# Kernel tuning notes

Hardware: AMD Instinct MI355X
Metric: run time of the kernel (lower is better)

Reference implementation:

```python
import jax, jax.numpy as jnp
import numpy as np

B, T, E, H, V = 64, 160, 512, 1024, 32000


def setup_inputs() -> dict:
    key = jax.random.key(0)
    ks = jax.random.split(key, 8)
    s = 1.0 / np.sqrt(H).astype(np.float32)
    return {
        "contexts": jax.random.randint(ks[0], (B, T), 0, V),
        "responses": jax.random.randint(ks[1], (B, T), 0, V),
        "emb": jax.random.normal(ks[2], (V, E), jnp.float32) * 0.02,
        "Wih": jax.random.uniform(ks[3], (4 * H, E), jnp.float32, -s, s),
        "Whh": jax.random.uniform(ks[4], (4 * H, H), jnp.float32, -s, s),
        "bih": jax.random.uniform(ks[5], (4 * H,), jnp.float32, -s, s),
        "bhh": jax.random.uniform(ks[6], (4 * H,), jnp.float32, -s, s),
        "M": jax.random.normal(ks[7], (H, H), jnp.float32),
    }


def _lstm_final_h(tokens, emb, Wih, Whh, bih, bhh):
    """Single-layer LSTM (PyTorch gate order i,f,g,o); returns final hidden state [B,H]."""
    x = emb[tokens]                      # [B, T, E]
    b = bih + bhh                        # [4H]
    hdim = Whh.shape[1]

    def step(carry, xt):
        h, c = carry
        gates = xt @ Wih.T + h @ Whh.T + b          # [B, 4H]
        i, f, g, o = jnp.split(gates, 4, axis=-1)
        c = jax.nn.sigmoid(f) * c + jax.nn.sigmoid(i) * jnp.tanh(g)
        h = jax.nn.sigmoid(o) * jnp.tanh(c)
        return (h, c), None

    h0 = jnp.zeros((tokens.shape[0], hdim), x.dtype)
    (h, _), _ = jax.lax.scan(step, (h0, h0), jnp.swapaxes(x, 0, 1))  # scan over time
    return h


def reference(contexts, responses, emb, Wih, Whh, bih, bhh, M):
    ch = _lstm_final_h(contexts, emb, Wih, Whh, bih, bhh)   # [B, H]
    rh = _lstm_final_h(responses, emb, Wih, Whh, bih, bhh)  # [B, H]
    # batched bilinear: sigmoid(diag(C @ M @ R^T)) -- replaces the per-example Python loop
    return jax.nn.sigmoid(jnp.einsum('bi,ij,bj->b', ch, M, rh))
```

## Files before the change

kernel.cpp:

```cpp
#include <hip/hip_runtime.h>
#include <math.h>


#define BB 64
#define TT 160
#define EE 512
#define HH 1024
#define G4 4096
#define ROWS 128
#define NB 256

typedef unsigned short u16;
typedef unsigned int u32;
typedef __attribute__((ext_vector_type(8))) __bf16 bf16x8;
typedef __attribute__((ext_vector_type(8))) short short8;
typedef __attribute__((ext_vector_type(4))) short short4v;
typedef __attribute__((ext_vector_type(4))) float f32x4;

__device__ __forceinline__ u16 f2b(float f) {
    unsigned u = __float_as_uint(f);
    u = u + 0x7fffu + ((u >> 16) & 1u);
    return (u16)(u >> 16);
}
__device__ __forceinline__ float b2f(u16 s) { return __uint_as_float(((unsigned)s) << 16); }

__device__ __forceinline__ f32x4 mfma16(short8 a, short8 b, f32x4 c) {
    return __builtin_amdgcn_mfma_f32_16x16x32_bf16(
        __builtin_bit_cast(bf16x8, a), __builtin_bit_cast(bf16x8, b), c, 0, 0, 0);
}

__device__ __forceinline__ void g2l16(const void* gsrc, void* ldst) {
    __builtin_amdgcn_global_load_lds(
        (const __attribute__((address_space(1))) u32*)gsrc,
        (__attribute__((address_space(3))) u32*)ldst, 16, 0, 0);
}

__global__ __launch_bounds__(256) void cvt_kernel(const float* __restrict__ in,
                                                  u16* __restrict__ out, int n4) {
    int i = blockIdx.x * 256 + threadIdx.x;
    if (i < n4) {
        f32x4 v = *(const f32x4*)(in + (size_t)i * 4);
        short4v o;
        o.x = (short)f2b(v.x); o.y = (short)f2b(v.y);
        o.z = (short)f2b(v.z); o.w = (short)f2b(v.w);
        *(short4v*)(out + (size_t)i * 4) = o;
    }
}

__global__ __launch_bounds__(256) void pre_gemm2(
    const int* __restrict__ ctx, const int* __restrict__ rsp,
    const u16* __restrict__ embb, const u16* __restrict__ Wihb,
    const float* __restrict__ bih, const float* __restrict__ bhh,
    u16* __restrict__ xg)
{
    __shared__ __align__(16) u16 As[2][128][64];
    __shared__ __align__(16) u16 Ws[2][128][64];
    __shared__ int toks[128];
    const int tid = threadIdx.x;
    const int n0 = blockIdx.x * 128;
    const int t  = blockIdx.y;

    if (tid < 128) {
        int r = tid;
        toks[tid] = (r < BB) ? ctx[r * TT + t] : rsp[(r - BB) * TT + t];
    }
    __syncthreads();

    const u16* asrc[4]; const u16* bsrc[4];
    #pragma unroll
    for (int q = 0; q < 4; ++q) {
        int i = tid + q * 256;
        int row = i >> 3, c16 = i & 7;
        int scol = ((c16 ^ (row & 7)) * 8);
        asrc[q] = embb + (size_t)toks[row] * EE + scol;
        bsrc[q] = Wihb + (size_t)(n0 + row) * EE + scol;
    }

    const int lane = tid & 63, wave = tid >> 6;
    const int wr = (wave >> 1) * 64, wc = (wave & 1) * 64;
    const int l15 = lane & 15, l4 = lane >> 4;
    f32x4 acc[4][4] = {};

    #pragma unroll
    for (int q = 0; q < 4; ++q) {
        g2l16(asrc[q], (char*)&As[0][0][0] + (tid + q * 256) * 16);
        g2l16(bsrc[q], (char*)&Ws[0][0][0] + (tid + q * 256) * 16);
    }
    for (int it = 0; it < 8; ++it) {
        __syncthreads();
        if (it + 1 < 8) {
            int kk = (it + 1) * 64, bs = (it + 1) & 1;
            #pragma unroll
            for (int q = 0; q < 4; ++q) {
                g2l16(asrc[q] + kk, (char*)&As[bs][0][0] + (tid + q * 256) * 16);
                g2l16(bsrc[q] + kk, (char*)&Ws[bs][0][0] + (tid + q * 256) * 16);
            }
        }
        const int b = it & 1;
        #pragma unroll
        for (int ks = 0; ks < 2; ++ks) {
            int c16 = ks * 4 + l4;
            short8 a[4], w[4];
            #pragma unroll
            for (int mf = 0; mf < 4; ++mf) {
                int R = wr + mf * 16 + l15;
                a[mf] = *(const short8*)((const char*)&As[b][0][0] + R * 128 + ((c16 ^ (R & 7)) << 4));
            }
            #pragma unroll
            for (int nf = 0; nf < 4; ++nf) {
                int Nn = wc + nf * 16 + l15;
                w[nf] = *(const short8*)((const char*)&Ws[b][0][0] + Nn * 128 + ((c16 ^ (Nn & 7)) << 4));
            }
            #pragma unroll
            for (int mf = 0; mf < 4; ++mf)
                #pragma unroll
                for (int nf = 0; nf < 4; ++nf)
                    acc[mf][nf] = mfma16(a[mf], w[nf], acc[mf][nf]);
        }
    }

    u16* xp = xg + (size_t)t * ROWS * G4;
    #pragma unroll
    for (int nf = 0; nf < 4; ++nf) {
        int n = n0 + wc + nf * 16 + l15;
        float bias = bih[n] + bhh[n];
        #pragma unroll
        for (int mf = 0; mf < 4; ++mf)
            #pragma unroll
            for (int q = 0; q < 4; ++q) {
                int r = wr + mf * 16 + l4 * 4 + q;
                xp[(size_t)r * G4 + n] = f2b(acc[mf][nf][q] + bias);
            }
    }
}

__global__ __launch_bounds__(512) void lstm_persist2(
    const u16* __restrict__ Whhb, const u16* __restrict__ xg,
    u16* __restrict__ hbuf, unsigned* __restrict__ bar)
{
    __shared__ float G[2][2][32][33];

    const int tid = threadIdx.x;
    const int bx = blockIdx.x;
    const int cg = bx & 127, rg = bx >> 7;
    const int r0 = rg * 64, j0 = cg * 8;

    const int lane = tid & 63, wave = tid >> 6;
    const int rsub = wave >> 2;
    const int kh   = wave & 3;
    const int l15 = lane & 15, l4 = lane >> 4;

    short8 breg[2][8];
    #pragma unroll
    for (int nf = 0; nf < 2; ++nf) {
        int c = nf * 16 + l15;
        int n = (c >> 3) * HH + j0 + (c & 7);
        const u16* wp = Whhb + (size_t)n * HH + kh * 256 + l4 * 8;
        #pragma unroll
        for (int ks = 0; ks < 8; ++ks)
            breg[nf][ks] = *(const short8*)(wp + ks * 32);
    }

    const int ur = tid >> 2;
    const int uj = (tid & 3) * 2;
    float c0 = 0.f, c1 = 0.f;

    __syncthreads();

    for (int t = 0; t < TT; ++t) {
        const u16* hin = hbuf + (size_t)(t & 1) * ROWS * HH;
        u16* hout      = hbuf + (size_t)((t + 1) & 1) * ROWS * HH;

        u32 xv[4] = {0, 0, 0, 0};
        if (tid < 256) {
            const u16* xp = xg + ((size_t)t * ROWS + r0 + ur) * G4 + j0 + uj;
            #pragma unroll
            for (int q = 0; q < 4; ++q) xv[q] = *(const u32*)(xp + q * HH);
        }

        const u16* abase = hin + (size_t)(r0 + rsub * 32 + l15) * HH + kh * 256 + l4 * 8;
        short8 a[2][8];
        #pragma unroll
        for (int half = 0; half < 2; ++half)
            #pragma unroll
            for (int ks = 0; ks < 8; ++ks)
                asm volatile("global_load_dwordx4 %0, %1, off sc0 sc1"
                             : "=v"(a[half][ks])
                             : "v"(abase + half * 16 * HH + ks * 32));
        asm volatile("s_waitcnt vmcnt(0)" ::: "memory");
        __builtin_amdgcn_sched_barrier(0);

        f32x4 acc[2][2] = {};
        #pragma unroll
        for (int ks = 0; ks < 8; ++ks) {
            acc[0][0] = mfma16(a[0][ks], breg[0][ks], acc[0][0]);
            acc[0][1] = mfma16(a[0][ks], breg[1][ks], acc[0][1]);
            acc[1][0] = mfma16(a[1][ks], breg[0][ks], acc[1][0]);
            acc[1][1] = mfma16(a[1][ks], breg[1][ks], acc[1][1]);
        }

        if (kh < 2) {
            #pragma unroll
            for (int mf = 0; mf < 2; ++mf)
                #pragma unroll
                for (int nf = 0; nf < 2; ++nf)
                    #pragma unroll
                    for (int q = 0; q < 4; ++q)
                        G[kh][rsub][mf * 16 + l4 * 4 + q][nf * 16 + l15] = acc[mf][nf][q];
        }
        __syncthreads();
        if (kh >= 2) {
            #pragma unroll
            for (int mf = 0; mf < 2; ++mf)
                #pragma unroll
                for (int nf = 0; nf < 2; ++nf)
                    #pragma unroll
                    for (int q = 0; q < 4; ++q)
                        G[kh - 2][rsub][mf * 16 + l4 * 4 + q][nf * 16 + l15] += acc[mf][nf][q];
        }
        __syncthreads();

        if (tid < 256) {
            const int rs = ur >> 5, rl = ur & 31;
            float g0[4], g1[4];
            #pragma unroll
            for (int q = 0; q < 4; ++q) {
                float x0 = b2f((u16)(xv[q] & 0xffffu));
                float x1 = b2f((u16)(xv[q] >> 16));
                g0[q] = G[0][rs][rl][q * 8 + uj]     + G[1][rs][rl][q * 8 + uj]     + x0;
                g1[q] = G[0][rs][rl][q * 8 + uj + 1] + G[1][rs][rl][q * 8 + uj + 1] + x1;
            }
            float i0 = 1.f / (1.f + expf(-g0[0])), i1 = 1.f / (1.f + expf(-g1[0]));
            float f0 = 1.f / (1.f + expf(-g0[1])), f1 = 1.f / (1.f + expf(-g1[1]));
            float t0 = tanhf(g0[2]),               t1 = tanhf(g1[2]);
            float o0 = 1.f / (1.f + expf(-g0[3])), o1 = 1.f / (1.f + expf(-g1[3]));
            c0 = f0 * c0 + i0 * t0;
            c1 = f1 * c1 + i1 * t1;
            float h0 = o0 * tanhf(c0), h1 = o1 * tanhf(c1);
            u32 hp = (u32)f2b(h0) | ((u32)f2b(h1) << 16);
            u16* hptr = hout + (size_t)(r0 + ur) * HH + j0 + uj;
            asm volatile("global_store_dword %0, %1, off sc0 sc1"
                         :: "v"(hptr), "v"(hp) : "memory");
        }

        if (t < TT - 1) {
            asm volatile("s_waitcnt vmcnt(0)" ::: "memory");
            __syncthreads();
            if (tid == 0) {
                __hip_atomic_fetch_add(bar, 1u, __ATOMIC_RELAXED, __HIP_MEMORY_SCOPE_AGENT);
                unsigned target = (unsigned)(t + 1) * (unsigned)NB;
                long spins = 0;
                while (__hip_atomic_load(bar, __ATOMIC_RELAXED, __HIP_MEMORY_SCOPE_AGENT) < target) {
                    __builtin_amdgcn_s_sleep(1);
                    if (++spins > 20000000L) break;
                }
            }
            __syncthreads();
            __builtin_amdgcn_sched_barrier(0);
        }
    }
}

template<int MODE>
__global__ __launch_bounds__(256) void step_fused(
    const int* __restrict__ ctx, const int* __restrict__ rsp,
    const u16* __restrict__ embb, const u16* __restrict__ Wihb,
    const u16* __restrict__ Whhb, const u16* __restrict__ xg,
    const float* __restrict__ bih, const float* __restrict__ bhh,
    const u16* __restrict__ hin, u16* __restrict__ hout,
    float* __restrict__ c_ws, int t)
{
    __shared__ __align__(16) u16 As[2][64][64];
    __shared__ __align__(16) u16 Ws[2][32][64];
    __shared__ float gs[64][32];
    __shared__ int toks[64];

    const int tid = threadIdx.x;
    const int cg = blockIdx.x & 127, rg = blockIdx.x >> 7;
    const int r0 = rg * 64, j0 = cg * 8;

    if (MODE == 1) {
        if (tid < 64) {
            int r = r0 + tid;
            toks[tid] = (r < BB) ? ctx[r * TT + t] : rsp[(r - BB) * TT + t];
        }
        __syncthreads();
    }

    const int arow0 = tid >> 3, c16a = tid & 7;
    const int arow1 = arow0 + 32;
    const int acol0 = ((c16a ^ (arow0 & 7)) * 8);
    const int acol1 = ((c16a ^ (arow1 & 7)) * 8);
    const u16* hA0 = hin + (size_t)(r0 + arow0) * HH + acol0;
    const u16* hA1 = hin + (size_t)(r0 + arow1) * HH + acol1;
    const u16* eA0 = nullptr; const u16* eA1 = nullptr;
    if (MODE == 1) {
        eA0 = embb + (size_t)toks[arow0] * EE + acol0;
        eA1 = embb + (size_t)toks[arow1] * EE + acol1;
    }
    const int nn = tid >> 3, c16b = tid & 7;
    const int bcol = ((c16b ^ (nn & 7)) * 8);
    const int wrow = (nn >> 3) * HH + j0 + (nn & 7);
    const u16* wHh = Whhb + (size_t)wrow * HH + bcol;
    const u16* wIh = (MODE == 1) ? (Wihb + (size_t)wrow * EE + bcol) : nullptr;

    const int NK = (MODE == 1) ? 24 : 16;

    auto stage = [&](int bs, int it) {
        int kk = it * 64;
        const u16 *s0, *s1, *sw;
        if (MODE == 1 && kk < EE) {
            s0 = eA0 + kk; s1 = eA1 + kk; sw = wIh + kk;
        } else {
            int khh = (MODE == 1) ? kk - EE : kk;
            s0 = hA0 + khh; s1 = hA1 + khh; sw = wHh + khh;
        }
        g2l16(s0, (char*)&As[bs][0][0] + tid * 16);
        g2l16(s1, (char*)&As[bs][0][0] + (tid + 256) * 16);
        g2l16(sw, (char*)&Ws[bs][0][0] + tid * 16);
    };

    const int lane = tid & 63, wave = tid >> 6;
    const int wr = wave * 16;
    const int l15 = lane & 15, l4 = lane >> 4;
    f32x4 acc[2] = {};

    stage(0, 0);
    for (int it = 0; it < NK; ++it) {
        __syncthreads();
        if (it + 1 < NK) stage((it + 1) & 1, it + 1);
        const int b = it & 1;
        #pragma unroll
        for (int ks = 0; ks < 2; ++ks) {
            int c16 = ks * 4 + l4;
            int R = wr + l15;
            short8 a = *(const short8*)((const char*)&As[b][0][0] + R * 128 + ((c16 ^ (R & 7)) << 4));
            #pragma unroll
            for (int nf = 0; nf < 2; ++nf) {
                int Nn = nf * 16 + l15;
                short8 w = *(const short8*)((const char*)&Ws[b][0][0] + Nn * 128 + ((c16 ^ (Nn & 7)) << 4));
                acc[nf] = mfma16(a, w, acc[nf]);
            }
        }
    }
    __syncthreads();
    #pragma unroll
    for (int nf = 0; nf < 2; ++nf)
        #pragma unroll
        for (int q = 0; q < 4; ++q)
            gs[wr + l4 * 4 + q][nf * 16 + l15] = acc[nf][q];
    __syncthreads();

    const int e = tid * 2;
    const int row = e >> 3, jj = e & 7;
    const int rglob = r0 + row;
    float g0[4], g1[4];
    #pragma unroll
    for (int g = 0; g < 4; ++g) { g0[g] = gs[row][g * 8 + jj]; g1[g] = gs[row][g * 8 + jj + 1]; }
    if (MODE == 2) {
        const u16* xp = xg + ((size_t)t * ROWS + rglob) * G4 + j0 + jj;
        #pragma unroll
        for (int g = 0; g < 4; ++g) { g0[g] += b2f(xp[g * HH]); g1[g] += b2f(xp[g * HH + 1]); }
    } else {
        #pragma unroll
        for (int g = 0; g < 4; ++g) {
            int n = g * HH + j0 + jj;
            g0[g] += bih[n] + bhh[n];
            g1[g] += bih[n + 1] + bhh[n + 1];
        }
    }
    size_t cidx = ((size_t)blockIdx.x * 64 + row) * 8 + jj;
    float c0 = c_ws[cidx], c1 = c_ws[cidx + 1];
    float i0 = 1.f / (1.f + expf(-g0[0])), i1 = 1.f / (1.f + expf(-g1[0]));
    float f0 = 1.f / (1.f + expf(-g0[1])), f1 = 1.f / (1.f + expf(-g1[1]));
    float t0 = tanhf(g0[2]),               t1 = tanhf(g1[2]);
    float o0 = 1.f / (1.f + expf(-g0[3])), o1 = 1.f / (1.f + expf(-g1[3]));
    float cn0 = f0 * c0 + i0 * t0;
    float cn1 = f1 * c1 + i1 * t1;
    c_ws[cidx] = cn0; c_ws[cidx + 1] = cn1;
    float h0 = o0 * tanhf(cn0), h1 = o1 * tanhf(cn1);
    unsigned hp = (unsigned)f2b(h0) | ((unsigned)f2b(h1) << 16);
    *(unsigned*)(hout + (size_t)rglob * HH + j0 + jj) = hp;
}

__global__ __launch_bounds__(256) void step_gemm_f32(
    const int* __restrict__ ctx, const int* __restrict__ rsp,
    const float* __restrict__ emb, const float* __restrict__ Wih, const float* __restrict__ Whh,
    const u16* __restrict__ hb, float* __restrict__ gates, int t)
{
    __shared__ __align__(16) u16 As[64][32];
    __shared__ __align__(16) u16 Ws[64][32];
    __shared__ int toks[64];
    const int tid = threadIdx.x;
    const int n0 = blockIdx.x * 64;
    const int r0 = blockIdx.y * 64;
    const int part = blockIdx.z;
    if (tid < 64) {
        int r = r0 + tid;
        toks[tid] = (r < BB) ? ctx[r * TT + t] : rsp[(r - BB) * TT + t];
    }
    __syncthreads();
    const int lane = tid & 63, wave = tid >> 6;
    const int wr = (wave >> 1) * 32, wc = (wave & 1) * 32;
    const int l15 = lane & 15, l4 = lane >> 4;
    f32x4 acc[2][2] = {};
    const int kstart = part * 768;
    const int srow = tid >> 2;
    const int sseg = (tid & 3) * 8;
    for (int it = 0; it < 24; ++it) {
        const int kg = kstart + it * 32;
        const int kk = kg + sseg;
        if (kg < EE) {
            const float* s = emb + (size_t)toks[srow] * EE + kk;
            #pragma unroll
            for (int q = 0; q < 8; ++q) As[srow][sseg + q] = f2b(s[q]);
            const float* sw = Wih + (size_t)(n0 + srow) * EE + kk;
            #pragma unroll
            for (int q = 0; q < 8; ++q) Ws[srow][sseg + q] = f2b(sw[q]);
        } else {
            *(short8*)&As[srow][sseg] = *(const short8*)(hb + (size_t)(r0 + srow) * HH + (kk - EE));
            const float* sw = Whh + (size_t)(n0 + srow) * HH + (kk - EE);
            #pragma unroll
            for (int q = 0; q < 8; ++q) Ws[srow][sseg + q] = f2b(sw[q]);
        }
        __syncthreads();
        #pragma unroll
        for (int mf = 0; mf < 2; ++mf)
            #pragma unroll
            for (int nf = 0; nf < 2; ++nf)
                acc[mf][nf] = mfma16(*(const short8*)&As[wr + mf * 16 + l15][l4 * 8],
                                     *(const short8*)&Ws[wc + nf * 16 + l15][l4 * 8], acc[mf][nf]);
        __syncthreads();
    }
    float* gp = gates + (size_t)part * ROWS * G4;
    #pragma unroll
    for (int mf = 0; mf < 2; ++mf)
        #pragma unroll
        for (int nf = 0; nf < 2; ++nf)
            #pragma unroll
            for (int q = 0; q < 4; ++q) {
                int r = r0 + wr + mf * 16 + l4 * 4 + q;
                int n = n0 + wc + nf * 16 + l15;
                gp[(size_t)r * G4 + n] = acc[mf][nf][q];
            }
}

__global__ __launch_bounds__(256) void lstm_update0(
    const float* __restrict__ gates, const float* __restrict__ bih, const float* __restrict__ bhh,
    u16* __restrict__ hb, float* __restrict__ c)
{
    int idx = blockIdx.x * 256 + threadIdx.x;
    int r = idx >> 8;
    int jj = (idx & 255) * 4;
    const float* gp0 = gates + (size_t)r * G4;
    const float* gp1 = gates + (size_t)(ROWS + r) * G4;
    float gate[4][4];
    #pragma unroll
    for (int g = 0; g < 4; ++g) {
        int n = g * HH + jj;
        f32x4 a = *(const f32x4*)(gp0 + n);
        f32x4 b = *(const f32x4*)(gp1 + n);
        #pragma unroll
        for (int q = 0; q < 4; ++q) gate[g][q] = a[q] + b[q] + bih[n + q] + bhh[n + q];
    }
    int cidx = r * HH + jj;
    f32x4 cv = *(const f32x4*)(c + cidx);
    f32x4 cn; short4v hn;
    #pragma unroll
    for (int q = 0; q < 4; ++q) {
        float si = 1.f / (1.f + expf(-gate[0][q]));
        float sf = 1.f / (1.f + expf(-gate[1][q]));
        float tg = tanhf(gate[2][q]);
        float so = 1.f / (1.f + expf(-gate[3][q]));
        float cval = sf * cv[q] + si * tg;
        cn[q] = cval;
        ((short*)&hn)[q] = (short)f2b(so * tanhf(cval));
    }
    *(f32x4*)(c + cidx) = cn;
    *(short4v*)(hb + cidx) = hn;
}

__global__ __launch_bounds__(256) void bilinear(
    const u16* __restrict__ hb, const float* __restrict__ M, float* __restrict__ out)
{
    int b = blockIdx.x;
    __shared__ float chs[HH];
    __shared__ float red[256];
    const u16* ch = hb + (size_t)b * HH;
    const u16* rh = hb + (size_t)(BB + b) * HH;
    for (int i = threadIdx.x; i < HH; i += 256) chs[i] = b2f(ch[i]);
    __syncthreads();
    float vj[4] = {0.f, 0.f, 0.f, 0.f};
    for (int i = 0; i < HH; ++i) {
        float chi = chs[i];
        const float* Mr = M + (size_t)i * HH;
        #pragma unroll
        for (int q = 0; q < 4; ++q) vj[q] += chi * Mr[threadIdx.x + q * 256];
    }
    float acc = 0.f;
    #pragma unroll
    for (int q = 0; q < 4; ++q) acc += vj[q] * b2f(rh[threadIdx.x + q * 256]);
    red[threadIdx.x] = acc;
    __syncthreads();
    for (int s = 128; s > 0; s >>= 1) {
        if (threadIdx.x < s) red[threadIdx.x] += red[threadIdx.x + s];
        __syncthreads();
    }
    if (threadIdx.x == 0) out[b] = 1.0f / (1.0f + expf(-red[0]));
}

extern "C" void kernel_launch(void* const* d_in, const int* in_sizes, int n_in,
                              void* d_out, int out_size, void* d_ws, size_t ws_size,
                              hipStream_t stream) {
    const int*   ctx = (const int*)d_in[0];
    const int*   rsp = (const int*)d_in[1];
    const float* emb = (const float*)d_in[2];
    const float* Wih = (const float*)d_in[3];
    const float* Whh = (const float*)d_in[4];
    const float* bih = (const float*)d_in[5];
    const float* bhh = (const float*)d_in[6];
    const float* M   = (const float*)d_in[7];
    float* out = (float*)d_out;

    char* w = (char*)d_ws;
    u16*   hbuf  = (u16*)w;   w += (size_t)2 * ROWS * HH * 2;
    float* c_ws  = (float*)w; w += (size_t)ROWS * HH * 4;
    float* gates = (float*)w; w += (size_t)2 * ROWS * G4 * 4;
    u16*   embb  = (u16*)w;   w += (size_t)32000 * EE * 2;
    u16*   Wihb  = (u16*)w;   w += (size_t)G4 * EE * 2;
    u16*   Whhb  = (u16*)w;   w += (size_t)G4 * HH * 2;
    unsigned* bar = (unsigned*)w; w += 256;
    size_t conv_need = (size_t)(w - (char*)d_ws);
    u16*   xg    = (u16*)w;   w += (size_t)TT * ROWS * G4 * 2;
    size_t xpre_need = (size_t)(w - (char*)d_ws);

    int mode = (ws_size >= xpre_need) ? 2 : (ws_size >= conv_need) ? 1 : 0;

    hipMemsetAsync(hbuf, 0, (size_t)2 * ROWS * HH * 2, stream);

    if (mode >= 1) {
        cvt_kernel<<<16000, 256, 0, stream>>>(emb, embb, 32000 * EE / 4);
        cvt_kernel<<<2048,  256, 0, stream>>>(Wih, Wihb, G4 * EE / 4);
        cvt_kernel<<<4096,  256, 0, stream>>>(Whh, Whhb, G4 * HH / 4);
    }

    if (mode == 2) {
        hipMemsetAsync(bar, 0, 256, stream);
        pre_gemm2<<<dim3(G4 / 128, TT), 256, 0, stream>>>(ctx, rsp, embb, Wihb, bih, bhh, xg);
        lstm_persist2<<<NB, 512, 0, stream>>>(Whhb, xg, hbuf, bar);
        bilinear<<<BB, 256, 0, stream>>>(hbuf, M, out);
    } else if (mode == 1) {
        hipMemsetAsync(c_ws, 0, (size_t)ROWS * HH * 4, stream);
        for (int t = 0; t < TT; ++t) {
            const u16* hin = hbuf + (size_t)(t & 1) * ROWS * HH;
            u16* hout      = hbuf + (size_t)((t + 1) & 1) * ROWS * HH;
            step_fused<1><<<256, 256, 0, stream>>>(ctx, rsp, embb, Wihb, Whhb, xg,
                                                   bih, bhh, hin, hout, c_ws, t);
        }
        bilinear<<<BB, 256, 0, stream>>>(hbuf, M, out);
    } else {
        hipMemsetAsync(c_ws, 0, (size_t)ROWS * HH * 4, stream);
        u16* hb = hbuf;
        dim3 sg(G4 / 64, ROWS / 64, 2);
        for (int t = 0; t < TT; ++t) {
            step_gemm_f32<<<sg, 256, 0, stream>>>(ctx, rsp, emb, Wih, Whh, hb, gates, t);
            lstm_update0<<<128, 256, 0, stream>>>(gates, bih, bhh, hb, c_ws);
        }
        bilinear<<<BB, 256, 0, stream>>>(hb, M, out);
    }
}
```

Baseline: 2.070 ms.

## Replace atomic grid barrier with per-block flags and row-group waits

Replaces the single global atomic counter barrier in the persistent LSTM kernel with per-block step flags. Each block polls only the 128 flags of its own row group using vector loads across a wavefront. It also moves the input-gate loads after the hidden-state loads so their latency overlaps the MFMA work. This relaxes the global synchronisation to the true dependency set and removes atomic contention. The cost is extra polling traffic and slightly out-of-range reads for the upper threads.

```diff
diff --git a/kernel.cpp b/kernel.cpp
--- a/kernel.cpp
+++ b/kernel.cpp
@@ -16,6 +16,7 @@
 typedef __attribute__((ext_vector_type(8))) short short8;
 typedef __attribute__((ext_vector_type(4))) short short4v;
 typedef __attribute__((ext_vector_type(4))) float f32x4;
+typedef __attribute__((ext_vector_type(4))) u32 u32x4;
 
 __device__ __forceinline__ u16 f2b(float f) {
     unsigned u = __float_as_uint(f);
@@ -134,9 +135,9 @@
     }
 }
 
-__global__ __launch_bounds__(512) void lstm_persist2(
+__global__ __launch_bounds__(512) void lstm_persist3(
     const u16* __restrict__ Whhb, const u16* __restrict__ xg,
-    u16* __restrict__ hbuf, unsigned* __restrict__ bar)
+    u16* __restrict__ hbuf, u32* __restrict__ flags)
 {
     __shared__ float G[2][2][32][33];
 
@@ -171,13 +172,6 @@
         const u16* hin = hbuf + (size_t)(t & 1) * ROWS * HH;
         u16* hout      = hbuf + (size_t)((t + 1) & 1) * ROWS * HH;
 
-        u32 xv[4] = {0, 0, 0, 0};
-        if (tid < 256) {
-            const u16* xp = xg + ((size_t)t * ROWS + r0 + ur) * G4 + j0 + uj;
-            #pragma unroll
-            for (int q = 0; q < 4; ++q) xv[q] = *(const u32*)(xp + q * HH);
-        }
-
         const u16* abase = hin + (size_t)(r0 + rsub * 32 + l15) * HH + kh * 256 + l4 * 8;
         short8 a[2][8];
         #pragma unroll
@@ -187,7 +181,16 @@
                 asm volatile("global_load_dwordx4 %0, %1, off sc0 sc1"
                              : "=v"(a[half][ks])
                              : "v"(abase + half * 16 * HH + ks * 32));
-        asm volatile("s_waitcnt vmcnt(0)" ::: "memory");
+
+        u32 xv0, xv1, xv2, xv3;
+        {
+            const u16* xp = xg + ((size_t)t * ROWS + r0 + ur) * G4 + j0 + uj;
+            asm volatile("global_load_dword %0, %1, off" : "=v"(xv0) : "v"(xp));
+            asm volatile("global_load_dword %0, %1, off" : "=v"(xv1) : "v"(xp + HH));
+            asm volatile("global_load_dword %0, %1, off" : "=v"(xv2) : "v"(xp + 2 * HH));
+            asm volatile("global_load_dword %0, %1, off" : "=v"(xv3) : "v"(xp + 3 * HH));
+        }
+        asm volatile("s_waitcnt vmcnt(4)" ::: "memory");
         __builtin_amdgcn_sched_barrier(0);
 
         f32x4 acc[2][2] = {};
@@ -220,9 +223,12 @@
         }
         __syncthreads();
 
+        asm volatile("s_waitcnt vmcnt(0)" ::: "memory");
+        __builtin_amdgcn_sched_barrier(0);
         if (tid < 256) {
             const int rs = ur >> 5, rl = ur & 31;
             float g0[4], g1[4];
+            u32 xv[4] = {xv0, xv1, xv2, xv3};
             #pragma unroll
             for (int q = 0; q < 4; ++q) {
                 float x0 = b2f((u16)(xv[q] & 0xffffu));
@@ -246,13 +252,24 @@
         if (t < TT - 1) {
             asm volatile("s_waitcnt vmcnt(0)" ::: "memory");
             __syncthreads();
+            const u32 target = (u32)(t + 1);
             if (tid == 0) {
-                __hip_atomic_fetch_add(bar, 1u, __ATOMIC_RELAXED, __HIP_MEMORY_SCOPE_AGENT);
-                unsigned target = (unsigned)(t + 1) * (unsigned)NB;
-                long spins = 0;
-                while (__hip_atomic_load(bar, __ATOMIC_RELAXED, __HIP_MEMORY_SCOPE_AGENT) < target) {
-                    __builtin_amdgcn_s_sleep(1);
-                    if (++spins > 20000000L) break;
+                asm volatile("global_store_dword %0, %1, off sc0 sc1"
+                             :: "v"(flags + bx), "v"(target) : "memory");
+            }
+            if (wave == 0) {
+                const u32* fp = flags + rg * 128 + (lane & 31) * 4;
+                int spins = 0;
+                while (true) {
+                    u32x4 fv;
+                    asm volatile("global_load_dwordx4 %0, %1, off sc0 sc1"
+                                 : "=v"(fv) : "v"(fp));
+                    asm volatile("s_waitcnt vmcnt(0)" ::: "memory");
+                    bool ok = (fv.x >= target) & (fv.y >= target) &
+                              (fv.z >= target) & (fv.w >= target);
+                    if (__all(ok)) break;
+                    __builtin_amdgcn_s_sleep(2);
+                    if (++spins > 4000000) break;
                 }
             }
             __syncthreads();
@@ -529,7 +546,7 @@
     u16*   embb  = (u16*)w;   w += (size_t)32000 * EE * 2;
     u16*   Wihb  = (u16*)w;   w += (size_t)G4 * EE * 2;
     u16*   Whhb  = (u16*)w;   w += (size_t)G4 * HH * 2;
-    unsigned* bar = (unsigned*)w; w += 256;
+    u32*   flags = (u32*)w;   w += 1024;
     size_t conv_need = (size_t)(w - (char*)d_ws);
     u16*   xg    = (u16*)w;   w += (size_t)TT * ROWS * G4 * 2;
     size_t xpre_need = (size_t)(w - (char*)d_ws);
@@ -545,9 +562,9 @@
     }
 
     if (mode == 2) {
-        hipMemsetAsync(bar, 0, 256, stream);
+        hipMemsetAsync(flags, 0, 1024, stream);
         pre_gemm2<<<dim3(G4 / 128, TT), 256, 0, stream>>>(ctx, rsp, embb, Wihb, bih, bhh, xg);
-        lstm_persist2<<<NB, 512, 0, stream>>>(Whhb, xg, hbuf, bar);
+        lstm_persist3<<<NB, 512, 0, stream>>>(Whhb, xg, hbuf, flags);
         bilinear<<<BB, 256, 0, stream>>>(hbuf, M, out);
     } else if (mode == 1) {
         hipMemsetAsync(c_ws, 0, (size_t)ROWS * HH * 4, stream);
```

Result: no change. 2.078 ms (+0.4%).
